# Kernel optimization log

Hardware: AMD Instinct MI355X
Metric: run time of the kernel (lower is better)

The kernel has to match this reference:

```python
import jax, jax.numpy as jnp
import numpy as np

EMB = 1024
HEADS = 16
HEAD_DIM = EMB // HEADS


def setup_inputs() -> dict:
    key = jax.random.key(0)
    ks = jax.random.split(key, 9)
    B, T = 2, 2048
    s = 1.0 / np.sqrt(EMB)
    x = jax.random.normal(ks[0], (B, T, EMB), dtype=jnp.float32)
    Wq = jax.random.normal(ks[1], (EMB, EMB), dtype=jnp.float32) * s
    bq = jnp.zeros((EMB,), dtype=jnp.float32)
    Wk = jax.random.normal(ks[2], (EMB, EMB), dtype=jnp.float32) * s
    bk = jnp.zeros((EMB,), dtype=jnp.float32)
    Wv = jax.random.normal(ks[3], (EMB, EMB), dtype=jnp.float32) * s
    bv = jnp.zeros((EMB,), dtype=jnp.float32)
    Wo = jax.random.normal(ks[4], (EMB, EMB), dtype=jnp.float32) * s
    bo = jnp.zeros((EMB,), dtype=jnp.float32)
    return {"x": x, "Wq": Wq, "bq": bq, "Wk": Wk, "bk": bk,
            "Wv": Wv, "bv": bv, "Wo": Wo, "bo": bo}


def reference(x, Wq, bq, Wk, bk, Wv, bv, Wo, bo):
    B, T, C = x.shape
    H, D = HEADS, HEAD_DIM
    # QKV projections -> (B, H, T, D)
    q = (x @ Wq + bq).reshape(B, T, H, D).transpose(0, 2, 1, 3)
    k = (x @ Wk + bk).reshape(B, T, H, D).transpose(0, 2, 1, 3)
    v = (x @ Wv + bv).reshape(B, T, H, D).transpose(0, 2, 1, 3)
    scores = jnp.einsum('bhqd,bhkd->bhqk', q, k) / np.sqrt(D).astype(np.float32)
    causal = jnp.tril(jnp.ones((T, T), dtype=bool))  # True where allowed
    scores = jnp.where(causal, scores, -jnp.inf)
    weights = jax.nn.softmax(scores, axis=-1)  # dropout is identity at eval
    out = jnp.einsum('bhqk,bhkd->bhqd', weights, v)
    out = out.transpose(0, 2, 1, 3).reshape(B, T, C)
    return out @ Wo + bo
```

## Files before the change

### kernel.cpp

```cpp
#include <hip/hip_runtime.h>

typedef unsigned short u16;
typedef u16 u16x8 __attribute__((ext_vector_type(8)));
typedef __bf16 bf16x8 __attribute__((ext_vector_type(8)));
typedef float f32x4 __attribute__((ext_vector_type(4)));

#define EMB 1024
#define TT 2048
#define BB 2
#define NHEADS 16
#define HD 64
#define MTOT (BB * TT)

__device__ __forceinline__ u16 cvt(float f) {
  return __builtin_bit_cast(u16, (__bf16)f);
}

__device__ __forceinline__ bf16x8 asbf(u16x8 v) {
  return __builtin_bit_cast(bf16x8, v);
}

__device__ __forceinline__ void gload16(const void* g, void* l) {
  __builtin_amdgcn_global_load_lds(
      (const __attribute__((address_space(1))) void*)g,
      (__attribute__((address_space(3))) void*)l, 16, 0, 0);
}

__global__ __launch_bounds__(256) void k_prep(
    const float* __restrict__ x, u16* __restrict__ xb,
    const float* __restrict__ W0, const float* __restrict__ W1,
    const float* __restrict__ W2, const float* __restrict__ W3,
    u16* __restrict__ T0, u16* __restrict__ T1, u16* __restrict__ T2,
    u16* __restrict__ T3) {
  __shared__ float tile[32][33];
  const int bid = blockIdx.x;
  const int tid = threadIdx.x;
  if (bid >= 4096) {
    int i = (bid - 4096) * 256 + tid;
    float4 a = ((const float4*)x)[i * 2];
    float4 b = ((const float4*)x)[i * 2 + 1];
    u16x8 o;
    o[0] = cvt(a.x); o[1] = cvt(a.y); o[2] = cvt(a.z); o[3] = cvt(a.w);
    o[4] = cvt(b.x); o[5] = cvt(b.y); o[6] = cvt(b.z); o[7] = cvt(b.w);
    ((u16x8*)xb)[i] = o;
    return;
  }
  const int z = bid >> 10;
  const float* __restrict__ W = (z == 0) ? W0 : (z == 1) ? W1 : (z == 2) ? W2 : W3;
  u16* __restrict__ Wt = (z == 0) ? T0 : (z == 1) ? T1 : (z == 2) ? T2 : T3;
  const int b = bid & 1023;
  const int bx = (b & 31) * 32, by = (b >> 5) * 32;
  const int tx = tid & 31;
  const int ty = tid >> 5;
#pragma unroll
  for (int r = ty; r < 32; r += 8) tile[r][tx] = W[(by + r) * EMB + bx + tx];
  __syncthreads();
  const int tx2 = tid & 15;
  const int ty2 = tid >> 4;
#pragma unroll
  for (int r = ty2; r < 32; r += 16) {
    unsigned v = (unsigned)cvt(tile[2 * tx2][r]) |
                 ((unsigned)cvt(tile[2 * tx2 + 1][r]) << 16);
    *(unsigned*)&Wt[(bx + r) * EMB + by + 2 * tx2] = v;
  }
}

__global__ __launch_bounds__(256) void k_gemm_qkv(
    const u16* __restrict__ xb, const u16* __restrict__ WqT,
    const u16* __restrict__ WkT, const u16* __restrict__ WvT,
    const float* __restrict__ bq, const float* __restrict__ bk,
    const float* __restrict__ bv, u16* __restrict__ Q, u16* __restrict__ K,
    u16* __restrict__ Vt) {
  __shared__ u16 Al[128 * 64];
  __shared__ u16 Bl[128 * 64];
  const int tid = threadIdx.x;
  const int lane = tid & 63;
  const int w = tid >> 6;
  const int wr = w >> 1, wc = w & 1;
  const int lr = lane & 15, lg = lane >> 4;
  const int m0 = blockIdx.x * 128;
  const int nb = blockIdx.y;
  const int seg = nb >> 3;
  const int n0 = (nb & 7) * 128;
  const u16* __restrict__ Bt = (seg == 0) ? WqT : (seg == 1) ? WkT : WvT;
  const float* __restrict__ bias = (seg == 0) ? bq : (seg == 1) ? bk : bv;

  f32x4 acc[4][4];
#pragma unroll
  for (int i = 0; i < 4; i++)
#pragma unroll
    for (int j = 0; j < 4; j++) acc[i][j] = (f32x4){0.f, 0.f, 0.f, 0.f};

  const int srow = tid >> 3;
  const int sgz = ((tid >> 3) & 3) | (((tid >> 6) & 1) << 2);
  const int sc = (tid & 7) ^ sgz;
  const u16* ga0 = xb + (m0 + srow) * EMB + sc * 8;
  const u16* gb0 = Bt + (n0 + srow) * EMB + sc * 8;
  char* la0 = (char*)Al + w * 1024;
  char* lb0 = (char*)Bl + w * 1024;
  const int gfr = (lr & 3) | (((lr >> 3) & 1) << 2);

  for (int k0 = 0; k0 < EMB; k0 += 64) {
#pragma unroll
    for (int m = 0; m < 4; m++) {
      gload16(ga0 + (32 * m) * EMB + k0, la0 + m * 4096);
      gload16(gb0 + (32 * m) * EMB + k0, lb0 + m * 4096);
    }
    __syncthreads();
    u16x8 af[4][2], bfr[4][2];
#pragma unroll
    for (int hh = 0; hh < 2; hh++) {
      const int pc = ((hh * 4 + lg) ^ gfr) * 16;
#pragma unroll
      for (int mi = 0; mi < 4; mi++)
        af[mi][hh] =
            *(const u16x8*)((char*)Al + (wr * 64 + mi * 16 + lr) * 128 + pc);
#pragma unroll
      for (int ni = 0; ni < 4; ni++)
        bfr[ni][hh] =
            *(const u16x8*)((char*)Bl + (wc * 64 + ni * 16 + lr) * 128 + pc);
    }
#pragma unroll
    for (int hh = 0; hh < 2; hh++)
#pragma unroll
      for (int mi = 0; mi < 4; mi++)
#pragma unroll
        for (int ni = 0; ni < 4; ni++)
          acc[mi][ni] = __builtin_amdgcn_mfma_f32_16x16x32_bf16(
              asbf(af[mi][hh]), asbf(bfr[ni][hh]), acc[mi][ni], 0, 0, 0);
    __syncthreads();
  }

#pragma unroll
  for (int mi = 0; mi < 4; mi++) {
    const int lmb = wr * 64 + mi * 16 + lg * 4;
#pragma unroll
    for (int ni = 0; ni < 4; ni++) {
      const int ln = wc * 64 + ni * 16 + lr;
      const int n = n0 + ln;
      const float bv_ = bias[n];
      const int h = n >> 6, d = n & 63;
#pragma unroll
      for (int r = 0; r < 4; r++) {
        const int m = m0 + lmb + r;
        const int b = m >> 11, t = m & 2047;
        float v = acc[mi][ni][r] + bv_;
        if (seg == 0) {
          v *= 0.18033688011f;
          Q[(((b * NHEADS + h) * TT) + t) * HD + d] = cvt(v);
        } else if (seg == 1) {
          K[(((b * NHEADS + h) * TT) + t) * HD + d] = cvt(v);
        } else {
          Vt[(((b * NHEADS + h) * HD) + d) * TT + t] = cvt(v);
        }
      }
    }
  }
}

__global__ __launch_bounds__(256) void k_attn(const u16* __restrict__ Q,
                                              const u16* __restrict__ Kg,
                                              const u16* __restrict__ Vt,
                                              u16* __restrict__ AO) {
  __shared__ u16 Kl[2][64 * 64];
  __shared__ u16 Vl[2][64 * 64];
  const int tid = threadIdx.x;
  const int lane = tid & 63;
  const int w = tid >> 6;
  const int lr = lane & 15, lg = lane >> 4;
  const int bh = blockIdx.x;
  const int pair = blockIdx.y;
  const int lo = pair, hi = 63 - pair;
  const int b32 = (w < 2) ? hi : lo;
  const int myend = b32 >> 1;
  const int q0 = b32 * 32 + (w & 1) * 16;
  const u16* __restrict__ Qh = Q + bh * TT * HD;
  const u16* __restrict__ Kh = Kg + bh * TT * HD;
  const u16* __restrict__ Vh = Vt + bh * HD * TT;

  const int srow = tid >> 3;
  const int sgz = ((tid >> 3) & 3) | (((tid >> 6) & 1) << 2);
  const int sc = (tid & 7) ^ sgz;

  u16x8 qf[2];
  qf[0] = *(const u16x8*)&Qh[(q0 + lr) * HD + lg * 8];
  qf[1] = *(const u16x8*)&Qh[(q0 + lr) * HD + 32 + lg * 8];

  f32x4 accO[4];
#pragma unroll
  for (int i = 0; i < 4; i++) accO[i] = (f32x4){0.f, 0.f, 0.f, 0.f};
  float mst = -__builtin_inff();
  float lsum = 0.f;

  const int nkt = (hi >> 1) + 1;

  gload16(Kh + srow * HD + sc * 8, (char*)Kl[0] + w * 1024);
  gload16(Kh + (srow + 32) * HD + sc * 8, (char*)Kl[0] + w * 1024 + 4096);
  gload16(Vh + srow * TT + sc * 8, (char*)Vl[0] + w * 1024);
  gload16(Vh + (srow + 32) * TT + sc * 8, (char*)Vl[0] + w * 1024 + 4096);
  __syncthreads();

  for (int kt = 0; kt < nkt; ++kt) {
    const int k0 = kt * 64;
    const int cur = kt & 1;
    if (kt + 1 < nkt) {
      const int kn = k0 + 64;
      char* kd = (char*)Kl[cur ^ 1] + w * 1024;
      char* vd = (char*)Vl[cur ^ 1] + w * 1024;
      gload16(Kh + (kn + srow) * HD + sc * 8, kd);
      gload16(Kh + (kn + srow + 32) * HD + sc * 8, kd + 4096);
      gload16(Vh + srow * TT + kn + sc * 8, vd);
      gload16(Vh + (srow + 32) * TT + kn + sc * 8, vd + 4096);
    }
    if (kt <= myend) {
      const char* Kc = (const char*)Kl[cur];
      const char* Vc = (const char*)Vl[cur];

      f32x4 s[4];
#pragma unroll
      for (int n = 0; n < 4; n++) s[n] = (f32x4){0.f, 0.f, 0.f, 0.f};
      __builtin_amdgcn_s_setprio(1);
#pragma unroll
      for (int n = 0; n < 4; n++) {
        const int kr =
            (lr & 3) + ((n & 1) << 2) + ((lr >> 2) << 3) + ((n >> 1) << 5);
        const int gg = (kr & 3) | (((kr >> 3) & 1) << 2);
#pragma unroll
        for (int dh = 0; dh < 2; dh++) {
          const int bo = ((dh * 4 + lg) ^ gg) << 4;
          u16x8 kf = *(const u16x8*)(Kc + kr * 128 + bo);
          s[n] = __builtin_amdgcn_mfma_f32_16x16x32_bf16(asbf(kf), asbf(qf[dh]),
                                                         s[n], 0, 0, 0);
        }
      }
      __builtin_amdgcn_s_setprio(0);
      if (kt == myend) {
        const int rowq = q0 + lr;
#pragma unroll
        for (int n = 0; n < 4; n++) {
          const int cb = k0 + ((n & 1) << 2) + (lg << 3) + ((n >> 1) << 5);
#pragma unroll
          for (int r = 0; r < 4; r++)
            if (cb + r > rowq) s[n][r] = -__builtin_inff();
        }
      }
      float m01 = fmaxf(fmaxf(s[0][0], s[0][1]), fmaxf(s[0][2], s[0][3]));
      float m1 = fmaxf(fmaxf(s[1][0], s[1][1]), fmaxf(s[1][2], s[1][3]));
      float m2 = fmaxf(fmaxf(s[2][0], s[2][1]), fmaxf(s[2][2], s[2][3]));
      float m3 = fmaxf(fmaxf(s[3][0], s[3][1]), fmaxf(s[3][2], s[3][3]));
      float lmax = fmaxf(fmaxf(m01, m1), fmaxf(m2, m3));
      if (!__all(lmax - mst <= 11.0f)) {
        float rm = lmax;
        rm = fmaxf(rm, __shfl_xor(rm, 16));
        rm = fmaxf(rm, __shfl_xor(rm, 32));
        float mnew = fmaxf(mst, rm);
        float corr = exp2f(mst - mnew);
        lsum *= corr;
        mst = mnew;
#pragma unroll
        for (int r = 0; r < 4; r++) {
          float ca = __shfl(corr, 20 * lg + r);
#pragma unroll
          for (int dt = 0; dt < 4; dt++) accO[dt][r] *= ca;
        }
      }
      float p[4][4];
      float ls = 0.f;
#pragma unroll
      for (int n = 0; n < 4; n++)
#pragma unroll
        for (int r = 0; r < 4; r++) {
          p[n][r] = exp2f(s[n][r] - mst);
          ls += p[n][r];
        }
      lsum += ls;
      u16x8 a1, a2;
#pragma unroll
      for (int r = 0; r < 4; r++) {
        a1[r] = cvt(p[0][r]);
        a1[4 + r] = cvt(p[1][r]);
        a2[r] = cvt(p[2][r]);
        a2[4 + r] = cvt(p[3][r]);
      }
      __builtin_amdgcn_s_setprio(1);
#pragma unroll
      for (int dt = 0; dt < 4; dt++) {
        const int row = dt * 16 + lr;
        const int gg = (row & 3) | (((row >> 3) & 1) << 2);
        const int bo0 = ((lg ^ gg) << 4);
        const int bo1 = (((4 + lg) ^ gg) << 4);
        u16x8 vf0 = *(const u16x8*)(Vc + row * 128 + bo0);
        u16x8 vf1 = *(const u16x8*)(Vc + row * 128 + bo1);
        accO[dt] = __builtin_amdgcn_mfma_f32_16x16x32_bf16(asbf(a1), asbf(vf0),
                                                           accO[dt], 0, 0, 0);
        accO[dt] = __builtin_amdgcn_mfma_f32_16x16x32_bf16(asbf(a2), asbf(vf1),
                                                           accO[dt], 0, 0, 0);
      }
      __builtin_amdgcn_s_setprio(0);
    }
    __syncthreads();
  }
  float t = lsum;
  t += __shfl_xor(t, 16);
  t += __shfl_xor(t, 32);
  float rinv = 1.0f / t;
  float ra[4];
#pragma unroll
  for (int r = 0; r < 4; r++) ra[r] = __shfl(rinv, 20 * lg + r);
  const int b = bh >> 4, h = bh & 15;
#pragma unroll
  for (int dt = 0; dt < 4; dt++)
#pragma unroll
    for (int r = 0; r < 4; r++) {
      const int row = q0 + lg * 4 + r;
      const int d = h * 64 + dt * 16 + lr;
      AO[(b * TT + row) * EMB + d] = cvt(accO[dt][r] * ra[r]);
    }
}

__global__ __launch_bounds__(256) void k_gemm_out(const u16* __restrict__ AO,
                                                  const u16* __restrict__ WoT,
                                                  const float* __restrict__ bo,
                                                  float* __restrict__ out) {
  __shared__ u16 Al[128 * 64];
  __shared__ u16 Bl[128 * 64];
  const int tid = threadIdx.x;
  const int lane = tid & 63;
  const int w = tid >> 6;
  const int wr = w >> 1, wc = w & 1;
  const int lr = lane & 15, lg = lane >> 4;
  const int m0 = blockIdx.x * 128;
  const int n0 = blockIdx.y * 128;

  f32x4 acc[4][4];
#pragma unroll
  for (int i = 0; i < 4; i++)
#pragma unroll
    for (int j = 0; j < 4; j++) acc[i][j] = (f32x4){0.f, 0.f, 0.f, 0.f};

  const int srow = tid >> 3;
  const int sgz = ((tid >> 3) & 3) | (((tid >> 6) & 1) << 2);
  const int sc = (tid & 7) ^ sgz;
  const u16* ga0 = AO + (m0 + srow) * EMB + sc * 8;
  const u16* gb0 = WoT + (n0 + srow) * EMB + sc * 8;
  char* la0 = (char*)Al + w * 1024;
  char* lb0 = (char*)Bl + w * 1024;
  const int gfr = (lr & 3) | (((lr >> 3) & 1) << 2);

  for (int k0 = 0; k0 < EMB; k0 += 64) {
#pragma unroll
    for (int m = 0; m < 4; m++) {
      gload16(ga0 + (32 * m) * EMB + k0, la0 + m * 4096);
      gload16(gb0 + (32 * m) * EMB + k0, lb0 + m * 4096);
    }
    __syncthreads();
    u16x8 af[4][2], bfr[4][2];
#pragma unroll
    for (int hh = 0; hh < 2; hh++) {
      const int pc = ((hh * 4 + lg) ^ gfr) * 16;
#pragma unroll
      for (int mi = 0; mi < 4; mi++)
        af[mi][hh] =
            *(const u16x8*)((char*)Al + (wr * 64 + mi * 16 + lr) * 128 + pc);
#pragma unroll
      for (int ni = 0; ni < 4; ni++)
        bfr[ni][hh] =
            *(const u16x8*)((char*)Bl + (wc * 64 + ni * 16 + lr) * 128 + pc);
    }
#pragma unroll
    for (int hh = 0; hh < 2; hh++)
#pragma unroll
      for (int mi = 0; mi < 4; mi++)
#pragma unroll
        for (int ni = 0; ni < 4; ni++)
          acc[mi][ni] = __builtin_amdgcn_mfma_f32_16x16x32_bf16(
              asbf(af[mi][hh]), asbf(bfr[ni][hh]), acc[mi][ni], 0, 0, 0);
    __syncthreads();
  }

#pragma unroll
  for (int mi = 0; mi < 4; mi++) {
    const int lmb = wr * 64 + mi * 16 + lg * 4;
#pragma unroll
    for (int ni = 0; ni < 4; ni++) {
      const int ln = wc * 64 + ni * 16 + lr;
      const int n = n0 + ln;
      const float bv_ = bo[n];
#pragma unroll
      for (int r = 0; r < 4; r++) {
        const int m = m0 + lmb + r;
        out[m * EMB + n] = acc[mi][ni][r] + bv_;
      }
    }
  }
}

extern "C" void kernel_launch(void* const* d_in, const int* in_sizes, int n_in,
                              void* d_out, int out_size, void* d_ws,
                              size_t ws_size, hipStream_t stream) {
  const float* x = (const float*)d_in[0];
  const float* Wq = (const float*)d_in[1];
  const float* bq = (const float*)d_in[2];
  const float* Wk = (const float*)d_in[3];
  const float* bk = (const float*)d_in[4];
  const float* Wv = (const float*)d_in[5];
  const float* bv = (const float*)d_in[6];
  const float* Wo = (const float*)d_in[7];
  const float* bo = (const float*)d_in[8];
  float* out = (float*)d_out;

  char* ws = (char*)d_ws;
  u16* xb = (u16*)ws;
  u16* WqT = (u16*)(ws + (8u << 20));
  u16* WkT = (u16*)(ws + (10u << 20));
  u16* WvT = (u16*)(ws + (12u << 20));
  u16* WoT = (u16*)(ws + (14u << 20));
  u16* Qb = (u16*)(ws + (16u << 20));
  u16* Kb = (u16*)(ws + (24u << 20));
  u16* Vtb = (u16*)(ws + (32u << 20));
  u16* AO = xb;

  k_prep<<<6144, 256, 0, stream>>>(x, xb, Wq, Wk, Wv, Wo, WqT, WkT, WvT, WoT);
  k_gemm_qkv<<<dim3(32, 24), 256, 0, stream>>>(xb, WqT, WkT, WvT, bq, bk, bv,
                                               Qb, Kb, Vtb);
  k_attn<<<dim3(32, 32), 256, 0, stream>>>(Qb, Kb, Vtb, AO);
  k_gemm_out<<<dim3(32, 8), 256, 0, stream>>>(AO, WoT, bo, out);
}
```

Before: 130.4 us.

## Vectorize GEMM epilogue stores via swapped MFMA operands and enlarge attention blocks

Swaps the MFMA A/B operands in the QKV (Q/K segments) and output GEMMs so each lane holds four consecutive columns, allowing packed ushort4/float4 stores and float4 bias loads instead of scalar scattered writes. The V-transpose path keeps the original layout but packs four consecutive t values per store. Separately, attention blocks grow to 512 threads covering 64-row query blocks (paired lo/hi), with each thread loading one K/V chunk per tile instead of two. The larger block may reduce occupancy and changes the causal load balance.

```diff
diff --git a/kernel.cpp b/kernel.cpp
--- a/kernel.cpp
+++ b/kernel.cpp
@@ -120,45 +120,72 @@
         bfr[ni][hh] =
             *(const u16x8*)((char*)Bl + (wc * 64 + ni * 16 + lr) * 128 + pc);
     }
-#pragma unroll
-    for (int hh = 0; hh < 2; hh++)
-#pragma unroll
-      for (int mi = 0; mi < 4; mi++)
-#pragma unroll
-        for (int ni = 0; ni < 4; ni++)
-          acc[mi][ni] = __builtin_amdgcn_mfma_f32_16x16x32_bf16(
-              asbf(af[mi][hh]), asbf(bfr[ni][hh]), acc[mi][ni], 0, 0, 0);
+    if (seg == 2) {
+#pragma unroll
+      for (int hh = 0; hh < 2; hh++)
+#pragma unroll
+        for (int mi = 0; mi < 4; mi++)
+#pragma unroll
+          for (int ni = 0; ni < 4; ni++)
+            acc[mi][ni] = __builtin_amdgcn_mfma_f32_16x16x32_bf16(
+                asbf(af[mi][hh]), asbf(bfr[ni][hh]), acc[mi][ni], 0, 0, 0);
+    } else {
+#pragma unroll
+      for (int hh = 0; hh < 2; hh++)
+#pragma unroll
+        for (int mi = 0; mi < 4; mi++)
+#pragma unroll
+          for (int ni = 0; ni < 4; ni++)
+            acc[mi][ni] = __builtin_amdgcn_mfma_f32_16x16x32_bf16(
+                asbf(bfr[ni][hh]), asbf(af[mi][hh]), acc[mi][ni], 0, 0, 0);
+    }
     __syncthreads();
   }
 
-#pragma unroll
-  for (int mi = 0; mi < 4; mi++) {
-    const int lmb = wr * 64 + mi * 16 + lg * 4;
+  const int b = m0 >> 11;
+  if (seg == 2) {
 #pragma unroll
     for (int ni = 0; ni < 4; ni++) {
-      const int ln = wc * 64 + ni * 16 + lr;
-      const int n = n0 + ln;
+      const int n = n0 + wc * 64 + ni * 16 + lr;
       const float bv_ = bias[n];
       const int h = n >> 6, d = n & 63;
-#pragma unroll
-      for (int r = 0; r < 4; r++) {
-        const int m = m0 + lmb + r;
-        const int b = m >> 11, t = m & 2047;
-        float v = acc[mi][ni][r] + bv_;
-        if (seg == 0) {
-          v *= 0.18033688011f;
-          Q[(((b * NHEADS + h) * TT) + t) * HD + d] = cvt(v);
-        } else if (seg == 1) {
-          K[(((b * NHEADS + h) * TT) + t) * HD + d] = cvt(v);
-        } else {
-          Vt[(((b * NHEADS + h) * HD) + d) * TT + t] = cvt(v);
-        }
-      }
-    }
-  }
-}
-
-__global__ __launch_bounds__(256) void k_attn(const u16* __restrict__ Q,
+      u16* vrow = Vt + (((b * NHEADS + h) * HD) + d) * TT;
+#pragma unroll
+      for (int mi = 0; mi < 4; mi++) {
+        const int t0 = (m0 + wr * 64 + mi * 16 + lg * 4) & 2047;
+        ushort4 pk;
+        pk.x = cvt(acc[mi][ni][0] + bv_);
+        pk.y = cvt(acc[mi][ni][1] + bv_);
+        pk.z = cvt(acc[mi][ni][2] + bv_);
+        pk.w = cvt(acc[mi][ni][3] + bv_);
+        *(ushort4*)&vrow[t0] = pk;
+      }
+    }
+  } else {
+    u16* __restrict__ dst = (seg == 0) ? Q : K;
+    const float qs = 0.18033688011f;
+#pragma unroll
+    for (int ni = 0; ni < 4; ni++) {
+      const int nbase = n0 + wc * 64 + ni * 16 + lg * 4;
+      const float4 bv4 = *(const float4*)&bias[nbase];
+      const int h = nbase >> 6, d0 = nbase & 63;
+#pragma unroll
+      for (int mi = 0; mi < 4; mi++) {
+        const int t = (m0 + wr * 64 + mi * 16 + lr) & 2047;
+        float v0 = acc[mi][ni][0] + bv4.x;
+        float v1 = acc[mi][ni][1] + bv4.y;
+        float v2 = acc[mi][ni][2] + bv4.z;
+        float v3 = acc[mi][ni][3] + bv4.w;
+        if (seg == 0) { v0 *= qs; v1 *= qs; v2 *= qs; v3 *= qs; }
+        ushort4 pk;
+        pk.x = cvt(v0); pk.y = cvt(v1); pk.z = cvt(v2); pk.w = cvt(v3);
+        *(ushort4*)&dst[(((b * NHEADS + h) * TT) + t) * HD + d0] = pk;
+      }
+    }
+  }
+}
+
+__global__ __launch_bounds__(512) void k_attn(const u16* __restrict__ Q,
                                               const u16* __restrict__ Kg,
                                               const u16* __restrict__ Vt,
                                               u16* __restrict__ AO) {
@@ -170,10 +197,10 @@
   const int lr = lane & 15, lg = lane >> 4;
   const int bh = blockIdx.x;
   const int pair = blockIdx.y;
-  const int lo = pair, hi = 63 - pair;
-  const int b32 = (w < 2) ? hi : lo;
-  const int myend = b32 >> 1;
-  const int q0 = b32 * 32 + (w & 1) * 16;
+  const int lo = pair, hi = 31 - pair;
+  const int qblk = (w < 4) ? hi : lo;
+  const int myend = qblk;
+  const int q0 = qblk * 64 + (w & 3) * 16;
   const u16* __restrict__ Qh = Q + bh * TT * HD;
   const u16* __restrict__ Kh = Kg + bh * TT * HD;
   const u16* __restrict__ Vh = Vt + bh * HD * TT;
@@ -192,12 +219,10 @@
   float mst = -__builtin_inff();
   float lsum = 0.f;
 
-  const int nkt = (hi >> 1) + 1;
+  const int nkt = hi + 1;
 
   gload16(Kh + srow * HD + sc * 8, (char*)Kl[0] + w * 1024);
-  gload16(Kh + (srow + 32) * HD + sc * 8, (char*)Kl[0] + w * 1024 + 4096);
   gload16(Vh + srow * TT + sc * 8, (char*)Vl[0] + w * 1024);
-  gload16(Vh + (srow + 32) * TT + sc * 8, (char*)Vl[0] + w * 1024 + 4096);
   __syncthreads();
 
   for (int kt = 0; kt < nkt; ++kt) {
@@ -205,12 +230,8 @@
     const int cur = kt & 1;
     if (kt + 1 < nkt) {
       const int kn = k0 + 64;
-      char* kd = (char*)Kl[cur ^ 1] + w * 1024;
-      char* vd = (char*)Vl[cur ^ 1] + w * 1024;
-      gload16(Kh + (kn + srow) * HD + sc * 8, kd);
-      gload16(Kh + (kn + srow + 32) * HD + sc * 8, kd + 4096);
-      gload16(Vh + srow * TT + kn + sc * 8, vd);
-      gload16(Vh + (srow + 32) * TT + kn + sc * 8, vd + 4096);
+      gload16(Kh + (kn + srow) * HD + sc * 8, (char*)Kl[cur ^ 1] + w * 1024);
+      gload16(Vh + srow * TT + kn + sc * 8, (char*)Vl[cur ^ 1] + w * 1024);
     }
     if (kt <= myend) {
       const char* Kc = (const char*)Kl[cur];
@@ -374,23 +395,23 @@
 #pragma unroll
         for (int ni = 0; ni < 4; ni++)
           acc[mi][ni] = __builtin_amdgcn_mfma_f32_16x16x32_bf16(
-              asbf(af[mi][hh]), asbf(bfr[ni][hh]), acc[mi][ni], 0, 0, 0);
+              asbf(bfr[ni][hh]), asbf(af[mi][hh]), acc[mi][ni], 0, 0, 0);
     __syncthreads();
   }
 
 #pragma unroll
-  for (int mi = 0; mi < 4; mi++) {
-    const int lmb = wr * 64 + mi * 16 + lg * 4;
-#pragma unroll
-    for (int ni = 0; ni < 4; ni++) {
-      const int ln = wc * 64 + ni * 16 + lr;
-      const int n = n0 + ln;
-      const float bv_ = bo[n];
-#pragma unroll
-      for (int r = 0; r < 4; r++) {
-        const int m = m0 + lmb + r;
-        out[m * EMB + n] = acc[mi][ni][r] + bv_;
-      }
+  for (int ni = 0; ni < 4; ni++) {
+    const int nbase = n0 + wc * 64 + ni * 16 + lg * 4;
+    const float4 bv4 = *(const float4*)&bo[nbase];
+#pragma unroll
+    for (int mi = 0; mi < 4; mi++) {
+      const int m = m0 + wr * 64 + mi * 16 + lr;
+      float4 v;
+      v.x = acc[mi][ni][0] + bv4.x;
+      v.y = acc[mi][ni][1] + bv4.y;
+      v.z = acc[mi][ni][2] + bv4.z;
+      v.w = acc[mi][ni][3] + bv4.w;
+      *(float4*)&out[m * EMB + nbase] = v;
     }
   }
 }
@@ -423,6 +444,6 @@
   k_prep<<<6144, 256, 0, stream>>>(x, xb, Wq, Wk, Wv, Wo, WqT, WkT, WvT, WoT);
   k_gemm_qkv<<<dim3(32, 24), 256, 0, stream>>>(xb, WqT, WkT, WvT, bq, bk, bv,
                                                Qb, Kb, Vtb);
-  k_attn<<<dim3(32, 32), 256, 0, stream>>>(Qb, Kb, Vtb, AO);
+  k_attn<<<dim3(32, 16), 512, 0, stream>>>(Qb, Kb, Vtb, AO);
   k_gemm_out<<<dim3(32, 8), 256, 0, stream>>>(AO, WoT, bo, out);
 }
```

Result: no change. 132.4 us (+1.5%).
